# Performance work log

Measured on AMD Instinct MI355X. Metric: run time of the kernel, lower is better.

The kernel has to match this reference:

```python
import jax, jax.numpy as jnp
import numpy as np

BATCH, SEQ, DIM = 2, 2048, 512
DEPTH, HEADS, DIM_HEAD = 4, 8, 64
DIM_COND = DIM * 4
FF_INNER = int(DIM * 4 * 2 / 3)  # 1365 (GEGLU inner dim)
SOFTCAP = 50.0


def _layernorm(x):  # no affine, eps matches torch LayerNorm
    mu = jnp.mean(x, axis=-1, keepdims=True)
    var = jnp.mean((x - mu) ** 2, axis=-1, keepdims=True)
    return (x - mu) * jax.lax.rsqrt(var + 1e-5)


def _rmsnorm(x, g):  # F.normalize(x, dim=-1) * sqrt(dim) * (g + 1)
    n = jnp.sqrt(jnp.sum(x * x, axis=-1, keepdims=True))
    return x / jnp.maximum(n, 1e-12) * (DIM ** 0.5) * (g + 1.0)


def setup_inputs() -> dict:
    key = jax.random.key(0)
    ks = jax.random.split(key, 32)
    rn = lambda k, shape, s=0.02: jax.random.normal(k, shape, jnp.float32) * s
    x = jax.random.normal(ks[0], (BATCH, SEQ, DIM), jnp.float32)
    times = jax.random.uniform(ks[1], (BATCH,), jnp.float32)
    attn_mask = jnp.broadcast_to(jnp.tril(jnp.ones((SEQ, SEQ), bool)), (BATCH, SEQ, SEQ))
    is_any_modality = jax.random.randint(ks[2], (BATCH, SEQ), 0, 2).astype(bool)
    D = DEPTH
    return dict(
        x=x, times=times, attn_mask=attn_mask, is_any_modality=is_any_modality,
        fourier_w=jax.random.normal(ks[3], (DIM // 2,), jnp.float32),
        time_w=rn(ks[4], (DIM + 1, DIM_COND)), time_b=rn(ks[5], (DIM_COND,)),
        aw_ln_g=rn(ks[6], (D, DIM)), aw_scale=jnp.ones((D, DIM), jnp.float32),
        aw_film_w=rn(ks[7], (D, DIM_COND, 2 * DIM)), aw_film_b=rn(ks[8], (D, 2 * DIM)),
        aw_zero_w=rn(ks[9], (D, DIM_COND, DIM)), aw_zero_b=jnp.full((D, DIM), -2.0, jnp.float32),
        attn_norm_g=rn(ks[10], (D, DIM)),
        qkv_w=rn(ks[11], (D, DIM, 3 * HEADS * DIM_HEAD)),
        out_w=rn(ks[12], (D, HEADS * DIM_HEAD, DIM)),
        fw_ln_g=rn(ks[13], (D, DIM)), fw_scale=jnp.ones((D, DIM), jnp.float32),
        fw_film_w=rn(ks[14], (D, DIM_COND, 2 * DIM)), fw_film_b=rn(ks[15], (D, 2 * DIM)),
        fw_zero_w=rn(ks[16], (D, DIM_COND, DIM)), fw_zero_b=jnp.full((D, DIM), -2.0, jnp.float32),
        ff_norm_g=rn(ks[17], (D, DIM)),
        ff_w1=rn(ks[18], (D, DIM, 2 * FF_INNER)), ff_b1=rn(ks[19], (D, 2 * FF_INNER)),
        ff_w2=rn(ks[20], (D, FF_INNER, DIM)), ff_b2=rn(ks[21], (D, DIM)),
        final_g=rn(ks[22], (DIM,)),
    )


def reference(x, times, attn_mask, is_any_modality, fourier_w, time_w, time_b,
              aw_ln_g, aw_scale, aw_film_w, aw_film_b, aw_zero_w, aw_zero_b,
              attn_norm_g, qkv_w, out_w,
              fw_ln_g, fw_scale, fw_film_w, fw_film_b, fw_zero_w, fw_zero_b,
              ff_norm_g, ff_w1, ff_b1, ff_w2, ff_b2, final_g):
    b, n, d = x.shape
    # time conditioning: RandomFourierEmbed -> Linear(dim+1, 4*dim) -> SiLU
    freqs = times[:, None] * fourier_w * (2.0 * jnp.pi)              # [b, d/2]
    femb = jnp.concatenate([times[:, None], jnp.sin(freqs), jnp.cos(freqs)], axis=-1)
    cond = jax.nn.silu(femb @ time_w + time_b)[:, None, :]           # [b, 1, 4d]
    mod = is_any_modality[..., None]                                  # [b, n, 1]
    neg = -jnp.finfo(x.dtype).max
    am = attn_mask[:, None, :, :]                                     # [b, 1, i, j]

    def adaptive(h, ln_g, lscale, film_w, film_b, zero_w, zero_b, fn):
        hn = _layernorm(h)
        gamma, beta = jnp.split(cond @ film_w + film_b, 2, axis=-1)
        xin = jnp.where(mod, hn * (gamma + 1.0) + beta, hn * (ln_g + 1.0))
        out = fn(xin)
        gate = jax.nn.sigmoid(cond @ zero_w + zero_b)
        return jnp.where(mod, out * gate, out * lscale)

    for l in range(DEPTH):
        def attn_fn(h, l=l):
            h = _rmsnorm(h, attn_norm_g[l])
            qkv = (h @ qkv_w[l]).reshape(b, n, 3, HEADS, DIM_HEAD)
            q, k, v = jnp.moveaxis(qkv, 2, 0)                         # each [b, n, h, dh]
            q = jnp.swapaxes(q, 1, 2) * (DIM_HEAD ** -0.5)            # [b, h, n, dh]
            k = jnp.swapaxes(k, 1, 2)
            v = jnp.swapaxes(v, 1, 2)
            sim = jnp.einsum('bhid,bhjd->bhij', q, k)
            sim = jnp.tanh(sim / SOFTCAP) * SOFTCAP                   # softclamp
            sim = jnp.where(am, sim, neg)
            attn = jax.nn.softmax(sim, axis=-1)
            o = jnp.einsum('bhij,bhjd->bhid', attn, v)
            o = jnp.swapaxes(o, 1, 2).reshape(b, n, HEADS * DIM_HEAD)
            return o @ out_w[l]

        def ff_fn(h, l=l):
            h = _rmsnorm(h, ff_norm_g[l])
            u = h @ ff_w1[l] + ff_b1[l]
            a, g = jnp.split(u, 2, axis=-1)
            return (jax.nn.gelu(g, approximate=False) * a) @ ff_w2[l] + ff_b2[l]

        x = adaptive(x, aw_ln_g[l], aw_scale[l], aw_film_w[l], aw_film_b[l], aw_zero_w[l], aw_zero_b[l], attn_fn) + x
        x = adaptive(x, fw_ln_g[l], fw_scale[l], fw_film_w[l], fw_film_b[l], fw_zero_w[l], fw_zero_b[l], ff_fn) + x

    return _rmsnorm(x, final_g)
```

## Files before the change

### kernel.cpp

```cpp
#include <hip/hip_runtime.h>
#include <hip/hip_bf16.h>

typedef unsigned short US;
typedef short short8 __attribute__((ext_vector_type(8)));
typedef float f32x4 __attribute__((ext_vector_type(4)));

__device__ __forceinline__ float bf2f(US u){ union{unsigned int i; float f;}x; x.i=((unsigned int)u)<<16; return x.f; }
__device__ __forceinline__ US f2bf(float f){ union{float f; unsigned int i;}x; x.f=f; return (US)((x.i + 0x7fffu + ((x.i>>16)&1u))>>16); }

__device__ __forceinline__ float fastrcp(float x){
#if __has_builtin(__builtin_amdgcn_rcpf)
    return __builtin_amdgcn_rcpf(x);
#else
    return 1.f/x;
#endif
}

__device__ __forceinline__ float wredsum(float v){
    #pragma unroll
    for (int off=1; off<64; off<<=1) v += __shfl_xor(v, off);
    return v;
}


__global__ void k_copy(const float* __restrict__ x, float* __restrict__ xf, int n){
    int i = blockIdx.x*256+threadIdx.x;
    if (i < n) xf[i] = x[i];
}

__global__ void k_f2b(const float* __restrict__ w, US* __restrict__ o, int n){
    int i = blockIdx.x*256+threadIdx.x;
    if (i < n) o[i] = f2bf(w[i]);
}

__global__ void k_detect(const int* __restrict__ p, int* flag){
    __shared__ int f;
    if (threadIdx.x==0) f=0;
    __syncthreads();
    int bad=0;
    for (int i=threadIdx.x;i<1024;i+=256) if (((unsigned)p[i])>1u) bad=1;
    if (bad) atomicOr(&f,1);
    __syncthreads();
    if (threadIdx.x==0) *flag=f;
}
__global__ void k_mod(const int* __restrict__ p, const int* __restrict__ flag, unsigned char* __restrict__ mod){
    int t = blockIdx.x*256+threadIdx.x;
    if (t<4096){
        int v = (*flag) ? (int)(((const unsigned char*)p)[t]) : p[t];
        mod[t] = v?1:0;
    }
}

__global__ void k_padw1(const float* __restrict__ w, US* __restrict__ wp){
    int i = blockIdx.x*256+threadIdx.x;
    if (i >= 4*512*2752) return;
    int n = i % 2752; int lk = i / 2752;
    wp[i] = (n<2730) ? f2bf(w[lk*2730 + n]) : (US)0;
}
__global__ void k_padb1(const float* __restrict__ b, float* __restrict__ bp){
    int i = blockIdx.x*256+threadIdx.x;
    if (i >= 4*2752) return;
    int n = i % 2752; int l = i / 2752;
    bp[i] = (n<2730) ? b[l*2730+n] : 0.f;
}
__global__ void k_padw2(const float* __restrict__ w, US* __restrict__ wp){
    int i = blockIdx.x*256+threadIdx.x;
    if (i >= 4*1376*512) return;
    int n = i % 512; int r = i / 512; int k = r % 1376; int l = r / 1376;
    wp[i] = (k<1365) ? f2bf(w[(l*1365+k)*512 + n]) : (US)0;
}

__global__ void k_femb(const float* __restrict__ times, const float* __restrict__ fw, float* __restrict__ femb){
    int i = blockIdx.x*256 + threadIdx.x;
    if (i >= 2*513) return;
    int b = i / 513, k = i % 513;
    float t = times[b];
    float val;
    if (k == 0) val = t;
    else if (k <= 256) val = sinf(t * fw[k-1] * 6.2831853071795865f);
    else val = cosf(t * fw[k-257] * 6.2831853071795865f);
    femb[i] = val;
}

__global__ __launch_bounds__(256) void k_cond1(const float* __restrict__ femb,
    const float* __restrict__ time_w, float* __restrict__ CACC)
{
    int wid = blockIdx.x*4 + (threadIdx.x>>6);
    int lane = threadIdx.x & 63;
    int kchunk = wid & 3;
    int colwave = wid >> 2;
    int j = ((colwave & 31) << 6) + lane;
    int b = colwave >> 5;
    int k0 = kchunk*129, k1 = k0+129; if (k1>513) k1=513;
    const float* fr = femb + b*513;
    float acc = 0.f;
    for (int k=k0;k<k1;++k) acc += fr[k]*time_w[(size_t)k*2048 + j];
    atomicAdd(&CACC[b*2048 + j], acc);
}
__global__ void k_condfin(const float* __restrict__ CACC, const float* __restrict__ time_b,
                          float* __restrict__ cond){
    int i = blockIdx.x*256+threadIdx.x;
    if (i>=4096) return;
    float v = CACC[i] + time_b[i & 2047];
    cond[i] = v/(1.f+expf(-v));
}

__global__ __launch_bounds__(256) void k_film1(
    const float* __restrict__ cond,
    const float* __restrict__ aw_film_w, const float* __restrict__ aw_zero_w,
    const float* __restrict__ fw_film_w, const float* __restrict__ fw_zero_w,
    float* __restrict__ FACC)
{
    int wid = blockIdx.x*4 + (threadIdx.x>>6);
    int lane = threadIdx.x & 63;
    int kchunk = wid & 3;
    int colwave = wid >> 2;
    int colinst0 = colwave << 6;
    int c = (colinst0 % 1536) + lane;
    int rest = colinst0 / 1536;
    int b = rest & 1;
    int lt = rest >> 1;
    int l = lt >> 1, t = lt & 1;
    const float* cr = cond + b*2048 + kchunk*512;
    const float* w; size_t stride;
    if (c < 1024){
        w = (t ? fw_film_w : aw_film_w) + (size_t)l*2048*1024 + (size_t)(kchunk*512)*1024 + c;
        stride = 1024;
    } else {
        w = (t ? fw_zero_w : aw_zero_w) + (size_t)l*2048*512 + (size_t)(kchunk*512)*512 + (c-1024);
        stride = 512;
    }
    float acc = 0.f;
    #pragma unroll 4
    for (int k=0;k<512;++k) acc += cr[k]*w[(size_t)k*stride];
    atomicAdd(&FACC[colinst0 + lane], acc);
}

__global__ void k_filmfin(const float* __restrict__ FACC,
    const float* __restrict__ aw_film_b, const float* __restrict__ aw_zero_b,
    const float* __restrict__ fw_film_b, const float* __restrict__ fw_zero_b,
    float* __restrict__ GAM, float* __restrict__ BET, float* __restrict__ GATE)
{
    int i = blockIdx.x*256+threadIdx.x;
    if (i >= 24576) return;
    int c = i % 1536; int rest = i/1536; int b = rest&1; int lt = rest>>1; int l = lt>>1, t = lt&1;
    float v = FACC[i];
    if (c < 1024){
        v += (t ? fw_film_b : aw_film_b)[l*1024 + c];
        if (c < 512) GAM[(lt*2+b)*512 + c] = v;
        else         BET[(lt*2+b)*512 + (c-512)] = v;
    } else {
        v += (t ? fw_zero_b : aw_zero_b)[l*512 + (c-1024)];
        GATE[(lt*2+b)*512 + (c-1024)] = 1.f/(1.f+expf(-v));
    }
}

__global__ __launch_bounds__(256) void k_normmod(
    const float* __restrict__ X, const float* __restrict__ gamma, const float* __restrict__ beta,
    const float* __restrict__ lng, const float* __restrict__ ng,
    const unsigned char* __restrict__ modv, US* __restrict__ Y)
{
    int token = blockIdx.x*4 + (threadIdx.x>>6);
    int lane = threadIdx.x & 63;
    int b = token >> 11;
    const float* xr = X + ((size_t)token<<9);
    float v[8], s=0.f;
    #pragma unroll
    for (int j=0;j<8;++j){ v[j]=xr[(j<<6)+lane]; s+=v[j]; }
    s = wredsum(s);
    float mu = s*(1.f/512.f);
    float vs = 0.f;
    #pragma unroll
    for (int j=0;j<8;++j){ float d=v[j]-mu; vs+=d*d; }
    vs = wredsum(vs);
    float rsig = rsqrtf(vs*(1.f/512.f)+1e-5f);
    int md = modv[token];
    float xin[8], ss=0.f;
    #pragma unroll
    for (int j=0;j<8;++j){
        int d = (j<<6)+lane;
        float hn = (v[j]-mu)*rsig;
        float xi = md ? hn*(gamma[(b<<9)+d]+1.f)+beta[(b<<9)+d] : hn*(lng[d]+1.f);
        xin[j]=xi; ss+=xi*xi;
    }
    ss = wredsum(ss);
    float fac = 22.62741699796952f / fmaxf(sqrtf(ss), 1e-12f);
    #pragma unroll
    for (int j=0;j<8;++j){
        int d=(j<<6)+lane;
        Y[((size_t)token<<9)+d] = f2bf(xin[j]*fac*(ng[d]+1.f));
    }
}

__global__ __launch_bounds__(256) void k_final(const float* __restrict__ X, const float* __restrict__ g, float* __restrict__ out){
    int token = blockIdx.x*4 + (threadIdx.x>>6);
    int lane = threadIdx.x & 63;
    const float* xr = X + ((size_t)token<<9);
    float v[8], ss=0.f;
    #pragma unroll
    for (int j=0;j<8;++j){ v[j]=xr[(j<<6)+lane]; ss+=v[j]*v[j]; }
    ss=wredsum(ss);
    float fac = 22.62741699796952f / fmaxf(sqrtf(ss),1e-12f);
    #pragma unroll
    for (int j=0;j<8;++j){
        int d=(j<<6)+lane;
        out[((size_t)token<<9)+d] = v[j]*fac*(g[d]+1.f);
    }
}

__global__ void k_act(const US* __restrict__ u, US* __restrict__ act){
    int idx = blockIdx.x*256+threadIdx.x;
    if (idx >= 4096*1376) return;
    int t = idx / 1376, c = idx % 1376;
    float val = 0.f;
    if (c < 1365) {
        float a = bf2f(u[t*2752 + c]);
        float g = bf2f(u[t*2752 + 1365 + c]);
        val = 0.5f*g*(1.f+erff(g*0.70710678118f)) * a;
    }
    act[idx] = f2bf(val);
}

template<int EPI>
__global__ __launch_bounds__(256) void k_gemm(
    const US* __restrict__ A, const US* __restrict__ Bm, US* __restrict__ C,
    const float* __restrict__ bias, float* __restrict__ X,
    const float* __restrict__ gate, const float* __restrict__ scale,
    const unsigned char* __restrict__ modv, int M, int N, int K)
{
    __shared__ US As[64*40];
    __shared__ US Bs[64*40];
    int tid = threadIdx.x;
    int wave = tid>>6, lane = tid&63, quad = lane>>4, l15 = lane&15;
    int m0 = blockIdx.y<<6, n0 = blockIdx.x<<6;
    f32x4 acc[4];
    #pragma unroll
    for (int nb=0;nb<4;++nb) acc[nb] = (f32x4){0.f,0.f,0.f,0.f};
    int arow = tid>>2, ac8 = (tid&3)<<3;
    int bn = tid&63, bk8 = (tid>>6)<<3;
    const US* Aptr = A + (size_t)(m0+arow)*K + ac8;
    const US* Bptr = Bm + n0 + bn;
    for (int k0=0;k0<K;k0+=32){
        __syncthreads();
        *(uint4*)&As[arow*40+ac8] = *(const uint4*)(Aptr + k0);
        {
            const US* bp = Bptr + (size_t)(k0+bk8)*N;
            unsigned int u0 = (unsigned int)bp[0]           | ((unsigned int)bp[(size_t)N]<<16);
            unsigned int u1 = (unsigned int)bp[2*(size_t)N] | ((unsigned int)bp[3*(size_t)N]<<16);
            unsigned int u2 = (unsigned int)bp[4*(size_t)N] | ((unsigned int)bp[5*(size_t)N]<<16);
            unsigned int u3 = (unsigned int)bp[6*(size_t)N] | ((unsigned int)bp[7*(size_t)N]<<16);
            uint4 wv; wv.x=u0; wv.y=u1; wv.z=u2; wv.w=u3;
            *(uint4*)&Bs[bn*40+bk8] = wv;
        }
        __syncthreads();
        short8 af = *(const short8*)&As[(wave*16+l15)*40 + (quad<<3)];
        #pragma unroll
        for (int nb=0;nb<4;++nb){
            short8 bf = *(const short8*)&Bs[((nb<<4)+l15)*40 + (quad<<3)];
            acc[nb] = __builtin_amdgcn_mfma_f32_16x16x32_bf16(af, bf, acc[nb], 0,0,0);
        }
    }
    #pragma unroll
    for (int nb=0;nb<4;++nb){
        int col = n0 + (nb<<4) + l15;
        #pragma unroll
        for (int r=0;r<4;++r){
            int row = m0 + wave*16 + (quad<<2) + r;
            float v = acc[nb][r];
            if (EPI==1 || EPI==3) v += bias[col];
            if (EPI<=1){
                C[(size_t)row*N + col] = f2bf(v);
            } else {
                float o = modv[row] ? v*gate[((row>>11)<<9) + col] : v*scale[col];
                X[((size_t)row<<9) + col] += o;
            }
        }
    }
}

__global__ __launch_bounds__(256) void k_vtrans(const US* __restrict__ qkv, US* __restrict__ VT){
    __shared__ US Ts[64*72];
    int bh = blockIdx.y;
    int kt = blockIdx.x;
    int b = bh>>3, h = bh&7;
    int tid = threadIdx.x;
    #pragma unroll
    for (int it=0; it<2; ++it){
        int idx = tid + (it<<8);
        int key = idx>>3, d8 = (idx&7)<<3;
        *(uint4*)&Ts[key*72 + d8] =
            *(const uint4*)(qkv + (size_t)(b*2048 + kt*64 + key)*1536 + 1024 + h*64 + d8);
    }
    __syncthreads();
    #pragma unroll
    for (int it=0; it<2; ++it){
        int oidx = tid + (it<<8);
        int d = oidx>>3, kb = (oidx&7)<<3;
        US tmp[8];
        #pragma unroll
        for (int j=0;j<8;++j) tmp[j] = Ts[(kb+j)*72 + d];
        *(uint4*)(VT + (size_t)bh*131072 + (size_t)d*2048 + kt*64 + kb) = *(uint4*)tmp;
    }
}

__global__ __launch_bounds__(256) void k_attn(const US* __restrict__ qkv, const US* __restrict__ VT,
                                              US* __restrict__ O)
{
    int blk = blockIdx.x;
    int bh = blk >> 4, p = blk & 15;
    int b = bh >> 3, h = bh & 7;
    int tid = threadIdx.x, wave = tid>>6, lane = tid&63, quad = lane>>4, l15 = lane&15;
    __shared__ US Ks[64*72];
    __shared__ US Vt[64*72];
    __shared__ US Ps[4*16*72];
    US* ps = Ps + wave*16*72;

    int skey0 = tid>>3,  soff0 = (tid&7)<<3;
    const US* Kg = qkv + (size_t)(b*2048)*1536 + 512 + h*64;
    const US* Vg = VT + (size_t)bh*131072;

    int rbs[2] = {p, 31-p};
    #pragma unroll
    for (int ti=0; ti<2; ++ti){
        int rb = rbs[ti];
        int qrow0 = (rb<<6) + (wave<<4);
        const US* qbase = qkv + (size_t)(b*2048 + qrow0 + l15)*1536 + h*64 + (quad<<3);
        short8 qf0 = *(const short8*)qbase;
        short8 qf1 = *(const short8*)(qbase + 32);
        f32x4 Oa[4];
        #pragma unroll
        for (int nb=0;nb<4;++nb) Oa[nb]=(f32x4){0.f,0.f,0.f,0.f};
        float lsum[4] = {0.f,0.f,0.f,0.f};

        uint4 ka0 = *(const uint4*)(Kg + (size_t)(skey0)*1536 + soff0);
        uint4 ka1 = *(const uint4*)(Kg + (size_t)(skey0+32)*1536 + soff0);
        uint4 va0 = *(const uint4*)(Vg + (size_t)(skey0)*2048 + soff0);
        uint4 va1 = *(const uint4*)(Vg + (size_t)(skey0+32)*2048 + soff0);

        for (int c=0; c<=rb; ++c){
            int j0 = c<<6;
            __syncthreads();
            *(uint4*)&Ks[skey0*72 + soff0]      = ka0;
            *(uint4*)&Ks[(skey0+32)*72 + soff0] = ka1;
            *(uint4*)&Vt[skey0*72 + soff0]      = va0;
            *(uint4*)&Vt[(skey0+32)*72 + soff0] = va1;
            __syncthreads();
            if (c < rb){
                int j1 = j0 + 64;
                ka0 = *(const uint4*)(Kg + (size_t)(j1+skey0)*1536 + soff0);
                ka1 = *(const uint4*)(Kg + (size_t)(j1+skey0+32)*1536 + soff0);
                va0 = *(const uint4*)(Vg + (size_t)(skey0)*2048 + j1 + soff0);
                va1 = *(const uint4*)(Vg + (size_t)(skey0+32)*2048 + j1 + soff0);
            }
            f32x4 s[4];
            #pragma unroll
            for (int nb=0;nb<4;++nb){
                s[nb]=(f32x4){0.f,0.f,0.f,0.f};
                short8 kf0 = *(const short8*)&Ks[((nb<<4)+l15)*72 + (quad<<3)];
                short8 kf1 = *(const short8*)&Ks[((nb<<4)+l15)*72 + 32 + (quad<<3)];
                s[nb] = __builtin_amdgcn_mfma_f32_16x16x32_bf16(qf0, kf0, s[nb],0,0,0);
                s[nb] = __builtin_amdgcn_mfma_f32_16x16x32_bf16(qf1, kf1, s[nb],0,0,0);
            }
            int diag = (c==rb);
            #pragma unroll
            for (int nb=0;nb<4;++nb){
                int grp = (nb<<1) + (l15>>3);
                #pragma unroll
                for (int r=0;r<4;++r){
                    float e2 = __expf(s[nb][r]*0.005f);
                    float t = 1.f - 2.f*fastrcp(e2+1.f);
                    float pv = __expf(50.f*t);
                    if (diag){
                        int key = j0 + (nb<<4) + l15;
                        int rowg = qrow0 + (quad<<2) + r;
                        if (key > rowg) pv = 0.f;
                    }
                    lsum[r] += pv;
                    ps[((quad<<2)+r)*72 + ((grp^r)<<3) + (l15&7)] = f2bf(pv);
                }
            }
            int gs0 = quad ^ (l15&3);
            int gs1 = (4+quad) ^ (l15&3);
            short8 pf0 = *(const short8*)&ps[l15*72 + (gs0<<3)];
            short8 pf1 = *(const short8*)&ps[l15*72 + (gs1<<3)];
            #pragma unroll
            for (int nb=0;nb<4;++nb){
                short8 vf0 = *(const short8*)&Vt[((nb<<4)+l15)*72 + (quad<<3)];
                short8 vf1 = *(const short8*)&Vt[((nb<<4)+l15)*72 + 32 + (quad<<3)];
                Oa[nb] = __builtin_amdgcn_mfma_f32_16x16x32_bf16(pf0, vf0, Oa[nb],0,0,0);
                Oa[nb] = __builtin_amdgcn_mfma_f32_16x16x32_bf16(pf1, vf1, Oa[nb],0,0,0);
            }
        }
        float inv[4];
        #pragma unroll
        for (int r=0;r<4;++r){
            float v = lsum[r];
            v += __shfl_xor(v,1); v += __shfl_xor(v,2);
            v += __shfl_xor(v,4); v += __shfl_xor(v,8);
            inv[r] = 1.f / fmaxf(v, 1e-30f);
        }
        #pragma unroll
        for (int nb=0;nb<4;++nb){
            #pragma unroll
            for (int r=0;r<4;++r){
                int rowg = qrow0 + (quad<<2) + r;
                O[(size_t)(b*2048+rowg)*512 + h*64 + (nb<<4) + l15] = f2bf(Oa[nb][r]*inv[r]);
            }
        }
    }
}

extern "C" void kernel_launch(void* const* d_in, const int* in_sizes, int n_in,
                              void* d_out, int out_size, void* d_ws, size_t ws_size,
                              hipStream_t stream)
{
    (void)in_sizes; (void)n_in; (void)out_size; (void)ws_size;
    const float* x        = (const float*)d_in[0];
    const float* times    = (const float*)d_in[1];
    const int*   mod_raw  = (const int*)d_in[3];
    const float* fourier  = (const float*)d_in[4];
    const float* time_w   = (const float*)d_in[5];
    const float* time_b   = (const float*)d_in[6];
    const float* aw_ln_g  = (const float*)d_in[7];
    const float* aw_scale = (const float*)d_in[8];
    const float* aw_film_w= (const float*)d_in[9];
    const float* aw_film_b= (const float*)d_in[10];
    const float* aw_zero_w= (const float*)d_in[11];
    const float* aw_zero_b= (const float*)d_in[12];
    const float* attn_norm_g=(const float*)d_in[13];
    const float* qkv_w    = (const float*)d_in[14];
    const float* out_w    = (const float*)d_in[15];
    const float* fw_ln_g  = (const float*)d_in[16];
    const float* fw_scale = (const float*)d_in[17];
    const float* fw_film_w= (const float*)d_in[18];
    const float* fw_film_b= (const float*)d_in[19];
    const float* fw_zero_w= (const float*)d_in[20];
    const float* fw_zero_b= (const float*)d_in[21];
    const float* ff_norm_g= (const float*)d_in[22];
    const float* ff_w1    = (const float*)d_in[23];
    const float* ff_b1    = (const float*)d_in[24];
    const float* ff_w2    = (const float*)d_in[25];
    const float* ff_b2    = (const float*)d_in[26];
    const float* final_g  = (const float*)d_in[27];

    char* ws = (char*)d_ws;
    size_t off = 0;
    auto alloc = [&](size_t bytes)->char*{ char* p = ws+off; off += (bytes + 255) & ~(size_t)255; return p; };
    float* Xf   = (float*)alloc(4096ull*512*4);
    US* Y       = (US*)alloc(4096ull*512*2);
    US* QKV     = (US*)alloc(4096ull*1536*2);
    US* VT      = (US*)alloc(16ull*64*2048*2);
    US* Ob      = (US*)alloc(4096ull*512*2);
    US* U       = (US*)alloc(4096ull*2752*2);
    US* ACT     = (US*)alloc(4096ull*1376*2);
    US* QW      = (US*)alloc(4ull*512*1536*2);
    US* OW      = (US*)alloc(4ull*512*512*2);
    US* W1P     = (US*)alloc(4ull*512*2752*2);
    float* B1P  = (float*)alloc(4ull*2752*4);
    US* W2P     = (US*)alloc(4ull*1376*512*2);
    float* FEMB = (float*)alloc(2*513*4);
    float* CACC = (float*)alloc(4096*4);
    float* COND = (float*)alloc(2*2048*4);
    float* FACC = (float*)alloc(24576*4);
    float* GAM  = (float*)alloc(8192*4);
    float* BET  = (float*)alloc(8192*4);
    float* GATE = (float*)alloc(8192*4);
    unsigned char* MOD = (unsigned char*)alloc(4096);
    int* FLAG   = (int*)alloc(256);

    k_copy<<<8192,256,0,stream>>>(x, Xf, 4096*512);
    k_detect<<<1,256,0,stream>>>(mod_raw, FLAG);
    k_mod<<<16,256,0,stream>>>(mod_raw, FLAG, MOD);
    k_f2b<<<(4*512*1536+255)/256,256,0,stream>>>(qkv_w, QW, 4*512*1536);
    k_f2b<<<(4*512*512+255)/256,256,0,stream>>>(out_w, OW, 4*512*512);
    k_padw1<<<(4*512*2752+255)/256,256,0,stream>>>(ff_w1, W1P);
    k_padb1<<<(4*2752+255)/256,256,0,stream>>>(ff_b1, B1P);
    k_padw2<<<(4*1376*512+255)/256,256,0,stream>>>(ff_w2, W2P);
    k_femb<<<5,256,0,stream>>>(times, fourier, FEMB);
    hipMemsetAsync(CACC, 0, 4096*4, stream);
    k_cond1<<<64,256,0,stream>>>(FEMB, time_w, CACC);
    k_condfin<<<16,256,0,stream>>>(CACC, time_b, COND);
    hipMemsetAsync(FACC, 0, 24576*4, stream);
    k_film1<<<384,256,0,stream>>>(COND, aw_film_w, aw_zero_w, fw_film_w, fw_zero_w, FACC);
    k_filmfin<<<96,256,0,stream>>>(FACC, aw_film_b, aw_zero_b, fw_film_b, fw_zero_b, GAM, BET, GATE);

    for (int l=0;l<4;++l){
        int lt0 = (l*2+0)*1024, lt1 = (l*2+1)*1024;
        k_normmod<<<1024,256,0,stream>>>(Xf, GAM+lt0, BET+lt0, aw_ln_g + l*512, attn_norm_g + l*512, MOD, Y);
        k_gemm<0><<<dim3(1536/64,64),256,0,stream>>>(Y, QW + (size_t)l*512*1536, QKV,
                    nullptr, nullptr, nullptr, nullptr, nullptr, 4096,1536,512);
        k_vtrans<<<dim3(32,16),256,0,stream>>>(QKV, VT);
        k_attn<<<256,256,0,stream>>>(QKV, VT, Ob);
        k_gemm<2><<<dim3(512/64,64),256,0,stream>>>(Ob, OW + (size_t)l*512*512, nullptr,
                    nullptr, Xf, GATE+lt0, aw_scale + l*512, MOD, 4096,512,512);
        k_normmod<<<1024,256,0,stream>>>(Xf, GAM+lt1, BET+lt1, fw_ln_g + l*512, ff_norm_g + l*512, MOD, Y);
        k_gemm<1><<<dim3(2752/64,64),256,0,stream>>>(Y, W1P + (size_t)l*512*2752, U,
                    B1P + l*2752, nullptr, nullptr, nullptr, nullptr, 4096,2752,512);
        k_act<<<(4096*1376+255)/256,256,0,stream>>>(U, ACT);
        k_gemm<3><<<dim3(512/64,64),256,0,stream>>>(ACT, W2P + (size_t)l*1376*512, nullptr,
                    ff_b2 + l*512, Xf, GATE+lt1, fw_scale + l*512, MOD, 4096,512,1376);
    }
    k_final<<<1024,256,0,stream>>>(Xf, final_g, (float*)d_out);
}
```

Baseline: 1.021 ms.

## Pre-transpose weights, enlarge GEMM tiles, use direct global-to-LDS loads, restructure FiLM

Weights are now converted to bf16 and transposed to N-major via a shared-memory transpose kernel, so the GEMM B-tile loads become contiguous 16-byte reads instead of strided 2-byte gathers. The GEMM moves from 64x64 tiles with one MFMA row per wave to 128xBN tiles where each wave computes a 64x(BN/2) sub-tile. Tiles are filled with global_load_lds straight into unpadded LDS, giving more reuse per load. The FiLM projections are split into two kernels that read float4 weights and compute both batch rows at once. Risks are LDS bank conflicts from dropping the padding, fewer blocks in the grid, and a padded FF inner dimension (2816) that adds some wasted compute.

```diff
diff --git a/kernel.cpp b/kernel.cpp
--- a/kernel.cpp
+++ b/kernel.cpp
@@ -16,6 +16,12 @@
 #endif
 }
 
+__device__ __forceinline__ void gload_lds16(const US* g, US* l){
+    __builtin_amdgcn_global_load_lds(
+        (const __attribute__((address_space(1))) unsigned int*)g,
+        (__attribute__((address_space(3))) unsigned int*)l, 16, 0, 0);
+}
+
 __device__ __forceinline__ float wredsum(float v){
     #pragma unroll
     for (int off=1; off<64; off<<=1) v += __shfl_xor(v, off);
@@ -26,11 +32,6 @@
 __global__ void k_copy(const float* __restrict__ x, float* __restrict__ xf, int n){
     int i = blockIdx.x*256+threadIdx.x;
     if (i < n) xf[i] = x[i];
-}
-
-__global__ void k_f2b(const float* __restrict__ w, US* __restrict__ o, int n){
-    int i = blockIdx.x*256+threadIdx.x;
-    if (i < n) o[i] = f2bf(w[i]);
 }
 
 __global__ void k_detect(const int* __restrict__ p, int* flag){
@@ -51,23 +52,41 @@
     }
 }
 
-__global__ void k_padw1(const float* __restrict__ w, US* __restrict__ wp){
-    int i = blockIdx.x*256+threadIdx.x;
-    if (i >= 4*512*2752) return;
-    int n = i % 2752; int lk = i / 2752;
-    wp[i] = (n<2730) ? f2bf(w[lk*2730 + n]) : (US)0;
-}
+__global__ __launch_bounds__(256) void k_wt(const float* __restrict__ src, US* __restrict__ dst,
+                                            int Ks, int N, int Kd, int Npad){
+    int l = blockIdx.z;
+    src += (size_t)l*Ks*N;
+    dst += (size_t)l*Npad*Kd;
+    __shared__ US T[64*65];
+    int k0 = blockIdx.x<<6, n0 = blockIdx.y<<6;
+    int tid = threadIdx.x;
+    #pragma unroll
+    for (int it=0; it<16; ++it){
+        int idx = (it<<8) + tid;
+        int r = idx>>6, c = idx&63;
+        int kk = k0+r, nn = n0+c;
+        float v = (kk<Ks && nn<N) ? src[(size_t)kk*N+nn] : 0.f;
+        T[c*65+r] = f2bf(v);
+    }
+    __syncthreads();
+    int g = tid&7, rr = tid>>3;
+    if (k0 + (g<<3) < Kd){
+        #pragma unroll
+        for (int half=0; half<2; ++half){
+            int nn = rr + (half<<5);
+            US tmp[8];
+            #pragma unroll
+            for (int j=0;j<8;++j) tmp[j] = T[nn*65 + (g<<3)+j];
+            *(uint4*)(dst + (size_t)(n0+nn)*Kd + k0 + (g<<3)) = *(uint4*)tmp;
+        }
+    }
+}
+
 __global__ void k_padb1(const float* __restrict__ b, float* __restrict__ bp){
     int i = blockIdx.x*256+threadIdx.x;
-    if (i >= 4*2752) return;
-    int n = i % 2752; int l = i / 2752;
+    if (i >= 4*2816) return;
+    int n = i % 2816; int l = i / 2816;
     bp[i] = (n<2730) ? b[l*2730+n] : 0.f;
-}
-__global__ void k_padw2(const float* __restrict__ w, US* __restrict__ wp){
-    int i = blockIdx.x*256+threadIdx.x;
-    if (i >= 4*1376*512) return;
-    int n = i % 512; int r = i / 512; int k = r % 1376; int l = r / 1376;
-    wp[i] = (k<1365) ? f2bf(w[(l*1365+k)*512 + n]) : (US)0;
 }
 
 __global__ void k_femb(const float* __restrict__ times, const float* __restrict__ fw, float* __restrict__ femb){
@@ -105,35 +124,59 @@
     cond[i] = v/(1.f+expf(-v));
 }
 
-__global__ __launch_bounds__(256) void k_film1(
-    const float* __restrict__ cond,
-    const float* __restrict__ aw_film_w, const float* __restrict__ aw_zero_w,
-    const float* __restrict__ fw_film_w, const float* __restrict__ fw_zero_w,
+__global__ __launch_bounds__(256) void k_film2f(const float* __restrict__ cond,
+    const float* __restrict__ aw_film_w, const float* __restrict__ fw_film_w,
     float* __restrict__ FACC)
 {
-    int wid = blockIdx.x*4 + (threadIdx.x>>6);
-    int lane = threadIdx.x & 63;
-    int kchunk = wid & 3;
-    int colwave = wid >> 2;
-    int colinst0 = colwave << 6;
-    int c = (colinst0 % 1536) + lane;
-    int rest = colinst0 / 1536;
-    int b = rest & 1;
-    int lt = rest >> 1;
-    int l = lt >> 1, t = lt & 1;
-    const float* cr = cond + b*2048 + kchunk*512;
-    const float* w; size_t stride;
-    if (c < 1024){
-        w = (t ? fw_film_w : aw_film_w) + (size_t)l*2048*1024 + (size_t)(kchunk*512)*1024 + c;
-        stride = 1024;
-    } else {
-        w = (t ? fw_zero_w : aw_zero_w) + (size_t)l*2048*512 + (size_t)(kchunk*512)*512 + (c-1024);
-        stride = 512;
-    }
-    float acc = 0.f;
+    __shared__ float cs[2][64];
+    int blk = blockIdx.x;
+    int lt = blk>>5, kc = blk&31;
+    int l = lt>>1, t = lt&1;
+    const float* W = (t? fw_film_w : aw_film_w) + (size_t)l*2048*1024 + ((size_t)(kc<<6))*1024;
+    int tid = threadIdx.x;
+    if (tid < 128) cs[tid>>6][tid&63] = cond[(tid>>6)*2048 + (kc<<6) + (tid&63)];
+    __syncthreads();
+    int c4 = tid<<2;
+    float a0=0,a1=0,a2=0,a3=0,b0=0,b1=0,b2=0,b3=0;
     #pragma unroll 4
-    for (int k=0;k<512;++k) acc += cr[k]*w[(size_t)k*stride];
-    atomicAdd(&FACC[colinst0 + lane], acc);
+    for (int k=0;k<64;++k){
+        float4 w = *(const float4*)&W[(size_t)k*1024 + c4];
+        float c0 = cs[0][k], c1 = cs[1][k];
+        a0 += c0*w.x; a1 += c0*w.y; a2 += c0*w.z; a3 += c0*w.w;
+        b0 += c1*w.x; b1 += c1*w.y; b2 += c1*w.z; b3 += c1*w.w;
+    }
+    float* F0 = &FACC[(lt*2+0)*1536 + c4];
+    float* F1 = &FACC[(lt*2+1)*1536 + c4];
+    atomicAdd(F0+0,a0); atomicAdd(F0+1,a1); atomicAdd(F0+2,a2); atomicAdd(F0+3,a3);
+    atomicAdd(F1+0,b0); atomicAdd(F1+1,b1); atomicAdd(F1+2,b2); atomicAdd(F1+3,b3);
+}
+
+__global__ __launch_bounds__(256) void k_film2z(const float* __restrict__ cond,
+    const float* __restrict__ aw_zero_w, const float* __restrict__ fw_zero_w,
+    float* __restrict__ FACC)
+{
+    __shared__ float cs[2][64];
+    int blk = blockIdx.x;
+    int lt = blk>>5, kc = blk&31;
+    int l = lt>>1, t = lt&1;
+    int tid = threadIdx.x;
+    if (tid < 128) cs[tid>>6][tid&63] = cond[(tid>>6)*2048 + (kc<<6) + (tid&63)];
+    __syncthreads();
+    int kh = tid>>7;
+    int c4 = (tid&127)<<2;
+    const float* W = (t? fw_zero_w : aw_zero_w) + (size_t)l*2048*512 + ((size_t)((kc<<6)+(kh<<5)))*512;
+    float a0=0,a1=0,a2=0,a3=0,b0=0,b1=0,b2=0,b3=0;
+    #pragma unroll 4
+    for (int k=0;k<32;++k){
+        float4 w = *(const float4*)&W[(size_t)k*512 + c4];
+        float c0 = cs[0][(kh<<5)+k], c1 = cs[1][(kh<<5)+k];
+        a0 += c0*w.x; a1 += c0*w.y; a2 += c0*w.z; a3 += c0*w.w;
+        b0 += c1*w.x; b1 += c1*w.y; b2 += c1*w.z; b3 += c1*w.w;
+    }
+    float* F0 = &FACC[(lt*2+0)*1536 + 1024 + c4];
+    float* F1 = &FACC[(lt*2+1)*1536 + 1024 + c4];
+    atomicAdd(F0+0,a0); atomicAdd(F0+1,a1); atomicAdd(F0+2,a2); atomicAdd(F0+3,a3);
+    atomicAdd(F1+0,b0); atomicAdd(F1+1,b1); atomicAdd(F1+2,b2); atomicAdd(F1+3,b3);
 }
 
 __global__ void k_filmfin(const float* __restrict__ FACC,
@@ -214,65 +257,76 @@
     int t = idx / 1376, c = idx % 1376;
     float val = 0.f;
     if (c < 1365) {
-        float a = bf2f(u[t*2752 + c]);
-        float g = bf2f(u[t*2752 + 1365 + c]);
+        float a = bf2f(u[(size_t)t*2816 + c]);
+        float g = bf2f(u[(size_t)t*2816 + 1365 + c]);
         val = 0.5f*g*(1.f+erff(g*0.70710678118f)) * a;
     }
     act[idx] = f2bf(val);
 }
 
-template<int EPI>
+template<int BN, int EPI>
 __global__ __launch_bounds__(256) void k_gemm(
-    const US* __restrict__ A, const US* __restrict__ Bm, US* __restrict__ C,
+    const US* __restrict__ A, const US* __restrict__ BT, US* __restrict__ C,
     const float* __restrict__ bias, float* __restrict__ X,
     const float* __restrict__ gate, const float* __restrict__ scale,
     const unsigned char* __restrict__ modv, int M, int N, int K)
 {
-    __shared__ US As[64*40];
-    __shared__ US Bs[64*40];
+    constexpr int BM = 128, BK = 32;
+    constexpr int NF = BN/32;
+    __shared__ US As[BM*BK];
+    __shared__ US Bs[BN*BK];
     int tid = threadIdx.x;
     int wave = tid>>6, lane = tid&63, quad = lane>>4, l15 = lane&15;
-    int m0 = blockIdx.y<<6, n0 = blockIdx.x<<6;
-    f32x4 acc[4];
-    #pragma unroll
-    for (int nb=0;nb<4;++nb) acc[nb] = (f32x4){0.f,0.f,0.f,0.f};
-    int arow = tid>>2, ac8 = (tid&3)<<3;
-    int bn = tid&63, bk8 = (tid>>6)<<3;
-    const US* Aptr = A + (size_t)(m0+arow)*K + ac8;
-    const US* Bptr = Bm + n0 + bn;
-    for (int k0=0;k0<K;k0+=32){
+    int m0 = blockIdx.y*BM, n0 = blockIdx.x*BN;
+    int wm = (wave&1)<<6;
+    int wn = (wave>>1)*(BN/2);
+    f32x4 acc[4][NF];
+    #pragma unroll
+    for (int i=0;i<4;++i)
+        #pragma unroll
+        for (int j=0;j<NF;++j) acc[i][j]=(f32x4){0.f,0.f,0.f,0.f};
+
+    const US* gA0 = A  + (size_t)(m0 + (tid>>2))*K + ((tid&3)<<3);
+    const US* gA1 = gA0 + (size_t)64*K;
+    const US* gB0 = BT + (size_t)(n0 + (tid>>2))*K + ((tid&3)<<3);
+    const US* gB1 = gB0 + (size_t)64*K;
+    US* lA0 = &As[tid<<3]; US* lA1 = &As[(tid<<3)+2048];
+    US* lB0 = &Bs[tid<<3]; US* lB1 = (BN==128)? &Bs[(tid<<3)+2048] : nullptr;
+
+    for (int k0=0; k0<K; k0+=BK){
         __syncthreads();
-        *(uint4*)&As[arow*40+ac8] = *(const uint4*)(Aptr + k0);
-        {
-            const US* bp = Bptr + (size_t)(k0+bk8)*N;
-            unsigned int u0 = (unsigned int)bp[0]           | ((unsigned int)bp[(size_t)N]<<16);
-            unsigned int u1 = (unsigned int)bp[2*(size_t)N] | ((unsigned int)bp[3*(size_t)N]<<16);
-            unsigned int u2 = (unsigned int)bp[4*(size_t)N] | ((unsigned int)bp[5*(size_t)N]<<16);
-            unsigned int u3 = (unsigned int)bp[6*(size_t)N] | ((unsigned int)bp[7*(size_t)N]<<16);
-            uint4 wv; wv.x=u0; wv.y=u1; wv.z=u2; wv.w=u3;
-            *(uint4*)&Bs[bn*40+bk8] = wv;
-        }
+        gload_lds16(gA0 + k0, lA0);
+        gload_lds16(gA1 + k0, lA1);
+        gload_lds16(gB0 + k0, lB0);
+        if (BN==128) gload_lds16(gB1 + k0, lB1);
         __syncthreads();
-        short8 af = *(const short8*)&As[(wave*16+l15)*40 + (quad<<3)];
-        #pragma unroll
-        for (int nb=0;nb<4;++nb){
-            short8 bf = *(const short8*)&Bs[((nb<<4)+l15)*40 + (quad<<3)];
-            acc[nb] = __builtin_amdgcn_mfma_f32_16x16x32_bf16(af, bf, acc[nb], 0,0,0);
-        }
-    }
-    #pragma unroll
-    for (int nb=0;nb<4;++nb){
-        int col = n0 + (nb<<4) + l15;
-        #pragma unroll
-        for (int r=0;r<4;++r){
-            int row = m0 + wave*16 + (quad<<2) + r;
-            float v = acc[nb][r];
-            if (EPI==1 || EPI==3) v += bias[col];
-            if (EPI<=1){
-                C[(size_t)row*N + col] = f2bf(v);
-            } else {
-                float o = modv[row] ? v*gate[((row>>11)<<9) + col] : v*scale[col];
-                X[((size_t)row<<9) + col] += o;
+        short8 af[4], bf[NF];
+        #pragma unroll
+        for (int i=0;i<4;++i) af[i] = *(const short8*)&As[(wm + (i<<4) + l15)*BK + (quad<<3)];
+        #pragma unroll
+        for (int j=0;j<NF;++j) bf[j] = *(const short8*)&Bs[(wn + (j<<4) + l15)*BK + (quad<<3)];
+        #pragma unroll
+        for (int i=0;i<4;++i)
+            #pragma unroll
+            for (int j=0;j<NF;++j)
+                acc[i][j] = __builtin_amdgcn_mfma_f32_16x16x32_bf16(af[i], bf[j], acc[i][j], 0,0,0);
+    }
+    #pragma unroll
+    for (int i=0;i<4;++i){
+        #pragma unroll
+        for (int j=0;j<NF;++j){
+            int col = n0 + wn + (j<<4) + l15;
+            #pragma unroll
+            for (int r=0;r<4;++r){
+                int row = m0 + wm + (i<<4) + (quad<<2) + r;
+                float v = acc[i][j][r];
+                if (EPI==1 || EPI==3) v += bias[col];
+                if (EPI<=1){
+                    C[(size_t)row*N + col] = f2bf(v);
+                } else {
+                    float o = modv[row] ? v*gate[((row>>11)<<9) + col] : v*scale[col];
+                    X[((size_t)row<<9) + col] += o;
+                }
             }
         }
     }
@@ -451,13 +505,13 @@
     US* QKV     = (US*)alloc(4096ull*1536*2);
     US* VT      = (US*)alloc(16ull*64*2048*2);
     US* Ob      = (US*)alloc(4096ull*512*2);
-    US* U       = (US*)alloc(4096ull*2752*2);
+    US* U       = (US*)alloc(4096ull*2816*2);
     US* ACT     = (US*)alloc(4096ull*1376*2);
-    US* QW      = (US*)alloc(4ull*512*1536*2);
-    US* OW      = (US*)alloc(4ull*512*512*2);
-    US* W1P     = (US*)alloc(4ull*512*2752*2);
-    float* B1P  = (float*)alloc(4ull*2752*4);
-    US* W2P     = (US*)alloc(4ull*1376*512*2);
+    US* QWT     = (US*)alloc(4ull*1536*512*2);
+    US* OWT     = (US*)alloc(4ull*512*512*2);
+    US* W1T     = (US*)alloc(4ull*2816*512*2);
+    float* B1P  = (float*)alloc(4ull*2816*4);
+    US* W2T     = (US*)alloc(4ull*512*1376*2);
     float* FEMB = (float*)alloc(2*513*4);
     float* CACC = (float*)alloc(4096*4);
     float* COND = (float*)alloc(2*2048*4);
@@ -471,33 +525,34 @@
     k_copy<<<8192,256,0,stream>>>(x, Xf, 4096*512);
     k_detect<<<1,256,0,stream>>>(mod_raw, FLAG);
     k_mod<<<16,256,0,stream>>>(mod_raw, FLAG, MOD);
-    k_f2b<<<(4*512*1536+255)/256,256,0,stream>>>(qkv_w, QW, 4*512*1536);
-    k_f2b<<<(4*512*512+255)/256,256,0,stream>>>(out_w, OW, 4*512*512);
-    k_padw1<<<(4*512*2752+255)/256,256,0,stream>>>(ff_w1, W1P);
-    k_padb1<<<(4*2752+255)/256,256,0,stream>>>(ff_b1, B1P);
-    k_padw2<<<(4*1376*512+255)/256,256,0,stream>>>(ff_w2, W2P);
+    k_wt<<<dim3(8,24,4),256,0,stream>>>(qkv_w, QWT, 512,1536, 512,1536);
+    k_wt<<<dim3(8,8,4),256,0,stream>>>(out_w, OWT, 512,512, 512,512);
+    k_wt<<<dim3(8,44,4),256,0,stream>>>(ff_w1, W1T, 512,2730, 512,2816);
+    k_wt<<<dim3(22,8,4),256,0,stream>>>(ff_w2, W2T, 1365,512, 1376,512);
+    k_padb1<<<(4*2816+255)/256,256,0,stream>>>(ff_b1, B1P);
     k_femb<<<5,256,0,stream>>>(times, fourier, FEMB);
     hipMemsetAsync(CACC, 0, 4096*4, stream);
     k_cond1<<<64,256,0,stream>>>(FEMB, time_w, CACC);
     k_condfin<<<16,256,0,stream>>>(CACC, time_b, COND);
     hipMemsetAsync(FACC, 0, 24576*4, stream);
-    k_film1<<<384,256,0,stream>>>(COND, aw_film_w, aw_zero_w, fw_film_w, fw_zero_w, FACC);
+    k_film2f<<<256,256,0,stream>>>(COND, aw_film_w, fw_film_w, FACC);
+    k_film2z<<<256,256,0,stream>>>(COND, aw_zero_w, fw_zero_w, FACC);
     k_filmfin<<<96,256,0,stream>>>(FACC, aw_film_b, aw_zero_b, fw_film_b, fw_zero_b, GAM, BET, GATE);
 
     for (int l=0;l<4;++l){
         int lt0 = (l*2+0)*1024, lt1 = (l*2+1)*1024;
         k_normmod<<<1024,256,0,stream>>>(Xf, GAM+lt0, BET+lt0, aw_ln_g + l*512, attn_norm_g + l*512, MOD, Y);
-        k_gemm<0><<<dim3(1536/64,64),256,0,stream>>>(Y, QW + (size_t)l*512*1536, QKV,
+        k_gemm<128,0><<<dim3(12,32),256,0,stream>>>(Y, QWT + (size_t)l*1536*512, QKV,
                     nullptr, nullptr, nullptr, nullptr, nullptr, 4096,1536,512);
         k_vtrans<<<dim3(32,16),256,0,stream>>>(QKV, VT);
         k_attn<<<256,256,0,stream>>>(QKV, VT, Ob);
-        k_gemm<2><<<dim3(512/64,64),256,0,stream>>>(Ob, OW + (size_t)l*512*512, nullptr,
+        k_gemm<64,2><<<dim3(8,32),256,0,stream>>>(Ob, OWT + (size_t)l*512*512, nullptr,
                     nullptr, Xf, GATE+lt0, aw_scale + l*512, MOD, 4096,512,512);
         k_normmod<<<1024,256,0,stream>>>(Xf, GAM+lt1, BET+lt1, fw_ln_g + l*512, ff_norm_g + l*512, MOD, Y);
-        k_gemm<1><<<dim3(2752/64,64),256,0,stream>>>(Y, W1P + (size_t)l*512*2752, U,
-                    B1P + l*2752, nullptr, nullptr, nullptr, nullptr, 4096,2752,512);
+        k_gemm<128,1><<<dim3(22,32),256,0,stream>>>(Y, W1T + (size_t)l*2816*512, U,
+                    B1P + l*2816, nullptr, nullptr, nullptr, nullptr, 4096,2816,512);
         k_act<<<(4096*1376+255)/256,256,0,stream>>>(U, ACT);
-        k_gemm<3><<<dim3(512/64,64),256,0,stream>>>(ACT, W2P + (size_t)l*1376*512, nullptr,
+        k_gemm<64,3><<<dim3(8,32),256,0,stream>>>(ACT, W2T + (size_t)l*512*1376, nullptr,
                     ff_b2 + l*512, Xf, GATE+lt1, fw_scale + l*512, MOD, 4096,512,1376);
     }
     k_final<<<1024,256,0,stream>>>(Xf, final_g, (float*)d_out);
```

New measurement: 965.8 us. -5.4%, faster.
